# Kernel tuning notes

Measured on AMD Instinct MI355X. Metric: run time of the kernel, lower is better.

Reference implementation:

```python
import jax, jax.numpy as jnp
import numpy as np
import math

L, D, H, V, B, S, MR = 8, 768, 12, 32000, 2, 1024, 4
HD = D // H

def setup_inputs() -> dict:
    key = jax.random.key(0)
    ks = iter(jax.random.split(key, 64))
    def rn(shape, s=0.02):
        return jax.random.normal(next(ks), shape, jnp.float32) * s
    inp = {}
    inp['tokens'] = jax.random.randint(next(ks), (B, S), 0, V, jnp.int32)
    inp['tok_emb'] = rn((V, D))
    inp['pos_emb'] = rn((S, D))
    for n in ['Wq_row', 'Wk_row', 'Wv_row', 'Wq_col', 'Wo']:
        inp[n] = rn((L, D, D))
    for n in ['bq_row', 'bk_row', 'bv_row', 'bq_col', 'bo']:
        inp[n] = jnp.zeros((L, D), jnp.float32)
    inp['ln1_g'] = jnp.ones((L, D), jnp.float32); inp['ln1_b'] = jnp.zeros((L, D), jnp.float32)
    inp['ln2_g'] = jnp.ones((L, D), jnp.float32); inp['ln2_b'] = jnp.zeros((L, D), jnp.float32)
    inp['W1'] = rn((L, D, MR * D)); inp['b1'] = jnp.zeros((L, MR * D), jnp.float32)
    inp['W2'] = rn((L, MR * D, D)); inp['b2'] = jnp.zeros((L, D), jnp.float32)
    inp['Wk_sh'] = rn((D, D)); inp['bk_sh'] = jnp.zeros((D,), jnp.float32)
    inp['Wv_sh'] = rn((D, D)); inp['bv_sh'] = jnp.zeros((D,), jnp.float32)
    inp['lnf_g'] = jnp.ones((D,), jnp.float32); inp['lnf_b'] = jnp.zeros((D,), jnp.float32)
    inp['Whead'] = rn((D, V)); inp['bhead'] = jnp.zeros((V,), jnp.float32)
    return inp

def _ln(x, g, b, eps=1e-5):
    m = x.mean(-1, keepdims=True)
    v = ((x - m) ** 2).mean(-1, keepdims=True)
    return (x - m) * jax.lax.rsqrt(v + eps) * g + b

def _heads(x):
    b, s, _ = x.shape
    return x.reshape(b, s, H, HD).transpose(0, 2, 1, 3)  # [B,H,S,hd]

def _merge(x):
    b, h, s, hd = x.shape
    return x.transpose(0, 2, 1, 3).reshape(b, s, h * hd)

def _forward(tokens, tok_emb, pos_emb, Wq_row, bq_row, Wk_row, bk_row, Wv_row, bv_row,
             Wq_col, bq_col, Wo, bo, ln1_g, ln1_b, ln2_g, ln2_b, W1, b1, W2, b2,
             Wk_sh, bk_sh, Wv_sh, bv_sh, lnf_g, lnf_b, Whead, bhead):
    s_len = tokens.shape[1]
    inv = 1.0 / math.sqrt(HD)
    x = tok_emb[tokens] + pos_emb[:s_len]
    mask = jnp.triu(jnp.ones((s_len, s_len), bool), 1)
    past_k, past_v = [], []
    for i in range(L):
        h = _ln(x, ln1_g[i], ln1_b[i])
        q_row = _heads(h @ Wq_row[i] + bq_row[i])
        k_row = _heads(h @ Wk_row[i] + bk_row[i])
        v_row = _heads(h @ Wv_row[i] + bv_row[i])
        q_col = _heads(h @ Wq_col[i] + bq_col[i])
        k_col = _heads(h @ Wk_sh + bk_sh)   # shared KV projector (archived memory)
        v_col = _heads(h @ Wv_sh + bv_sh)
        ts = jnp.einsum('bhqd,bhkd->bhqk', q_row, k_row) * inv
        ts = jnp.where(mask, -jnp.inf, ts)
        if past_k:
            pk = jnp.stack(past_k, axis=3)  # [B,H,S,l,hd]
            pv = jnp.stack(past_v, axis=3)
            ms = jnp.einsum('bhsd,bhsld->bhsl', q_col, pk) * inv
            w = jax.nn.softmax(jnp.concatenate([ts, ms], axis=-1), axis=-1)
            tw, mw = w[..., :s_len], w[..., s_len:]
            ctx = (jnp.einsum('bhqk,bhkd->bhqd', tw, v_row)
                   + jnp.einsum('bhsl,bhsld->bhsd', mw, pv))
        else:
            ctx = jnp.einsum('bhqk,bhkd->bhqd', jax.nn.softmax(ts, axis=-1), v_row)
        x = x + (_merge(ctx) @ Wo[i] + bo[i])
        h2 = _ln(x, ln2_g[i], ln2_b[i])
        x = x + (jax.nn.gelu(h2 @ W1[i] + b1[i], approximate=False) @ W2[i] + b2[i])
        past_k.append(k_col)
        past_v.append(v_col)
    return _ln(x, lnf_g, lnf_b) @ Whead + bhead

def reference(tokens, tok_emb, pos_emb, Wq_row, bq_row, Wk_row, bk_row, Wv_row, bv_row,
              Wq_col, bq_col, Wo, bo, ln1_g, ln1_b, ln2_g, ln2_b, W1, b1, W2, b2,
              Wk_sh, bk_sh, Wv_sh, bv_sh, lnf_g, lnf_b, Whead, bhead):
    return _forward(tokens, tok_emb, pos_emb, Wq_row, bq_row, Wk_row, bk_row, Wv_row, bv_row,
                    Wq_col, bq_col, Wo, bo, ln1_g, ln1_b, ln2_g, ln2_b, W1, b1, W2, b2,
                    Wk_sh, bk_sh, Wv_sh, bv_sh, lnf_g, lnf_b, Whead, bhead)
```

## Files before the change

### kernel.cpp

```cpp
#include <hip/hip_runtime.h>
#include <hip/hip_bf16.h>
#include <math.h>

#define L_   8
#define D_   768
#define H_   12
#define V_   32000
#define B_   2
#define S_   1024
#define HD_  64
#define BS_  2048
#define DFF_ 3072

typedef __hip_bfloat16 bf16;
typedef __attribute__((ext_vector_type(8))) short bf16x8;
typedef __attribute__((ext_vector_type(4))) float f32x4;

#define CFUN(r) (((r) >> 1) & 3)

__device__ __forceinline__ void cp16(void* lds, const void* g) {
  __builtin_amdgcn_global_load_lds(
      (const __attribute__((address_space(1))) void*)g,
      (__attribute__((address_space(3))) void*)lds, 16, 0, 0);
}

__device__ __forceinline__ unsigned short f2bf(float v) {
  __hip_bfloat16 h = __float2bfloat16(v);
  return *reinterpret_cast<unsigned short*>(&h);
}
__device__ __forceinline__ float bf2f(unsigned short u) {
  return __uint_as_float(((unsigned)u) << 16);
}

__global__ __launch_bounds__(256) void k_embed(const int* __restrict__ tokens,
    const float* __restrict__ tok_emb, const float* __restrict__ pos_emb,
    float* __restrict__ x) {
  int idx = blockIdx.x * 256 + threadIdx.x;
  int row = idx / D_;
  int d   = idx - row * D_;
  int s   = row & (S_ - 1);
  int t   = tokens[row];
  x[idx] = tok_emb[(size_t)t * D_ + d] + pos_emb[(size_t)s * D_ + d];
}

__global__ __launch_bounds__(256) void k_ln(const float* __restrict__ x,
    const float* __restrict__ g, const float* __restrict__ b,
    bf16* __restrict__ out) {
  int row = blockIdx.x;
  const float* xr = x + (size_t)row * D_;
  int t = threadIdx.x;
  float v0 = xr[t], v1 = xr[t + 256], v2 = xr[t + 512];
  float s  = v0 + v1 + v2;
  float s2 = v0 * v0 + v1 * v1 + v2 * v2;
#pragma unroll
  for (int off = 32; off; off >>= 1) {
    s  += __shfl_down(s, off);
    s2 += __shfl_down(s2, off);
  }
  __shared__ float rs[4], rs2[4];
  __shared__ float mean_s, rstd_s;
  int wid = t >> 6;
  if ((t & 63) == 0) { rs[wid] = s; rs2[wid] = s2; }
  __syncthreads();
  if (t == 0) {
    float S1 = rs[0] + rs[1] + rs[2] + rs[3];
    float S2 = rs2[0] + rs2[1] + rs2[2] + rs2[3];
    float m  = S1 / D_;
    float var = S2 / D_ - m * m;
    mean_s = m;
    rstd_s = rsqrtf(var + 1e-5f);
  }
  __syncthreads();
  float m = mean_s, r = rstd_s;
  bf16* orow = out + (size_t)row * D_;
  orow[t]       = __float2bfloat16((v0 - m) * r * g[t]       + b[t]);
  orow[t + 256] = __float2bfloat16((v1 - m) * r * g[t + 256] + b[t + 256]);
  orow[t + 512] = __float2bfloat16((v2 - m) * r * g[t + 512] + b[t + 512]);
}

__global__ __launch_bounds__(256) void k_w2bf_t(const float* __restrict__ W,
    bf16* __restrict__ Wt, int K, int N, size_t ils, size_t ols) {
  __shared__ float t[32][33];
  const float* Wm = W + (size_t)blockIdx.z * ils;
  bf16* Wtm = Wt + (size_t)blockIdx.z * ols;
  int n0 = blockIdx.x * 32, k0 = blockIdx.y * 32;
  int tx = threadIdx.x;
  for (int i = threadIdx.y; i < 32; i += 8)
    t[i][tx] = Wm[(size_t)(k0 + i) * N + n0 + tx];
  __syncthreads();
  for (int i = threadIdx.y; i < 32; i += 8)
    Wtm[(size_t)(n0 + i) * K + k0 + tx] = __float2bfloat16(t[tx][i]);
}

__global__ __launch_bounds__(256) void k_bcat(const float* __restrict__ bq,
    const float* __restrict__ bk, const float* __restrict__ bqc,
    const float* __restrict__ bv, const float* __restrict__ bksh,
    const float* __restrict__ bvsh, float* __restrict__ b6) {
  int idx = blockIdx.x * 256 + threadIdx.x;
  if (idx >= L_ * 4608) return;
  int l = idx / 4608, c = idx - l * 4608;
  float v = (c < 768)  ? bq[l * 768 + c]
          : (c < 1536) ? bk[l * 768 + c - 768]
          : (c < 2304) ? bqc[l * 768 + c - 1536]
          : (c < 3072) ? bv[l * 768 + c - 2304]
          : (c < 3840) ? bksh[c - 3072]
                       : bvsh[c - 3840];
  b6[idx] = v;
}

template <int BM, int EPI>
__global__ __launch_bounds__(256) void k_bgemm(
    const bf16* __restrict__ A, const bf16* __restrict__ Wt,
    const float* __restrict__ bias, const float* __restrict__ resid,
    float* __restrict__ Cf, bf16* __restrict__ Cb, bf16* __restrict__ Cb2,
    bf16* __restrict__ Cb3, int NM, int M, int N, int K) {
  constexpr int ASZ = BM * 64;
  constexpr int ALINES = BM / 64;
  constexpr int BSTRIDE = ASZ + 8192;
  constexpr int MF = BM / 32;
  __shared__ __align__(16) char smem[3 * BSTRIDE];
  const int tid = threadIdx.x;
  const int l = tid & 63, w = tid >> 6;
  const int wr = w >> 1, wc = w & 1;

  const int nwg = (int)gridDim.x;
  int id = (int)blockIdx.x;
  id = (id & 7) * (nwg >> 3) + (id >> 3);
  const int m0 = (id % NM) * BM;
  const int n0 = (id / NM) * 128;

  const int lane15 = l & 15, lg = l >> 4;

  const int r0 = tid >> 2, p0 = tid & 3;
  const char* aSrc[ALINES];
#pragma unroll
  for (int i = 0; i < ALINES; i++) {
    const int rr = i * 64 + r0;
    aSrc[i] = (const char*)(A + (size_t)(m0 + rr) * K) + ((p0 ^ CFUN(rr)) * 16);
  }
  const char* bSrc0 = (const char*)(Wt + (size_t)(n0 + r0) * K) + ((p0 ^ CFUN(r0)) * 16);
  const char* bSrc1 = (const char*)(Wt + (size_t)(n0 + 64 + r0) * K) + ((p0 ^ CFUN(64 + r0)) * 16);

  int aOff[MF], bOff[4];
#pragma unroll
  for (int mi = 0; mi < MF; mi++) {
    int r = wr * (BM / 2) + mi * 16 + lane15;
    aOff[mi] = r * 64 + ((lg ^ CFUN(r)) * 16);
  }
#pragma unroll
  for (int ni = 0; ni < 4; ni++) {
    int r = wc * 64 + ni * 16 + lane15;
    bOff[ni] = ASZ + r * 64 + ((lg ^ CFUN(r)) * 16);
  }

  f32x4 acc[MF][4];
#pragma unroll
  for (int mi = 0; mi < MF; mi++)
#pragma unroll
    for (int ni = 0; ni < 4; ni++) acc[mi][ni] = (f32x4){0.f, 0.f, 0.f, 0.f};

  auto stage = [&](int buf, int t) {
    const size_t kb = (size_t)t * 64;
    char* base = smem + buf * BSTRIDE;
#pragma unroll
    for (int i = 0; i < ALINES; i++)
      cp16(base + i * 4096 + w * 1024, aSrc[i] + kb);
    cp16(base + ASZ + w * 1024, bSrc0 + kb);
    cp16(base + ASZ + 4096 + w * 1024, bSrc1 + kb);
  };
  auto compute = [&](int buf) {
    const char* base = smem + buf * BSTRIDE;
    bf16x8 af[MF], bfr[4];
#pragma unroll
    for (int mi = 0; mi < MF; mi++) af[mi] = *(const bf16x8*)(base + aOff[mi]);
#pragma unroll
    for (int ni = 0; ni < 4; ni++) bfr[ni] = *(const bf16x8*)(base + bOff[ni]);
    __builtin_amdgcn_s_setprio(1);
#pragma unroll
    for (int mi = 0; mi < MF; mi++)
#pragma unroll
      for (int ni = 0; ni < 4; ni++)
        acc[mi][ni] = __builtin_amdgcn_mfma_f32_16x16x32_bf16(
            af[mi], bfr[ni], acc[mi][ni], 0, 0, 0);
    __builtin_amdgcn_s_setprio(0);
  };

  const int nk = K >> 5;
  stage(0, 0);
  stage(1, 1);
  int buf = 0;
  for (int t = 0; t < nk; t++) {
    if (t + 1 < nk) {
      if constexpr (ALINES == 2) asm volatile("s_waitcnt vmcnt(4)" ::: "memory");
      else                       asm volatile("s_waitcnt vmcnt(3)" ::: "memory");
    } else {
      asm volatile("s_waitcnt vmcnt(0)" ::: "memory");
    }
    __builtin_amdgcn_s_barrier();
    if (t + 2 < nk) {
      int nb = buf + 2; if (nb >= 3) nb -= 3;
      stage(nb, t + 2);
    }
    compute(buf);
    buf = (buf == 2) ? 0 : buf + 1;
  }

#pragma unroll
  for (int ni = 0; ni < 4; ni++) {
    const int col = n0 + wc * 64 + ni * 16 + lane15;
    const float bv = bias[col];
#pragma unroll
    for (int mi = 0; mi < MF; mi++) {
      const int rowb = m0 + wr * (BM / 2) + mi * 16 + lg * 4;
      if constexpr (EPI == 6) {
        if (col < 2304) {
#pragma unroll
          for (int j = 0; j < 4; j++)
            Cb[(size_t)(rowb + j) * 2304 + col] = __float2bfloat16(acc[mi][ni][j] + bv);
        } else if (col < 3072) {
          ushort4 pk;
          pk.x = f2bf(acc[mi][ni][0] + bv);
          pk.y = f2bf(acc[mi][ni][1] + bv);
          pk.z = f2bf(acc[mi][ni][2] + bv);
          pk.w = f2bf(acc[mi][ni][3] + bv);
          const int bq = rowb >> 10, s = rowb & (S_ - 1);
          *reinterpret_cast<ushort4*>(
              (unsigned short*)Cb2 + ((size_t)(bq * 768 + (col - 2304))) * S_ + s) = pk;
        } else {
#pragma unroll
          for (int j = 0; j < 4; j++)
            Cb3[(size_t)(rowb + j) * 1536 + (col - 3072)] =
                __float2bfloat16(acc[mi][ni][j] + bv);
        }
      } else {
#pragma unroll
        for (int j = 0; j < 4; j++) {
          const int row = rowb + j;
          float v = acc[mi][ni][j] + bv;
          if constexpr (EPI == 1) v += resid[(size_t)row * N + col];
          if constexpr (EPI == 2) {
            v = 0.5f * v * (1.0f + erff(v * 0.70710678118654752f));
            Cb[(size_t)row * N + col] = __float2bfloat16(v);
          } else if constexpr (EPI == 3) {
            Cb[(size_t)row * N + col] = __float2bfloat16(v);
          } else {
            Cf[(size_t)row * N + col] = v;
          }
        }
      }
    }
  }
}

__global__ __launch_bounds__(256) void k_attn(
    const bf16* __restrict__ qkv, const bf16* __restrict__ vT,
    const bf16* __restrict__ memkv, bf16* __restrict__ ctx, int layer) {
  const int bh = blockIdx.x;
  const int b = bh / H_, h = bh % H_;
  const int qt = (int)gridDim.y - 1 - (int)blockIdx.y;
  const int tid = threadIdx.x;
  const int w = tid >> 6, l = tid & 63;
  const int lane15 = l & 15, lg = l >> 4;
  const float inv = 0.125f;

  __shared__ char plds[4][2048];
  __shared__ float wlp[4][16][16];
  char* pl = plds[w];

  const int qrow0 = qt * 64 + w * 16;
  const size_t rowA = (size_t)(b * S_ + qrow0 + lane15);
  const bf16* qp = qkv + rowA * 2304 + h * 64 + lg * 8;
  const bf16x8 qf0 = *(const bf16x8*)(qp);
  const bf16x8 qf1 = *(const bf16x8*)(qp + 32);

  const bf16* kbase = qkv + (size_t)(b * S_) * 2304 + 768 + h * 64 + lg * 8;
  const bf16* vbase = vT + ((size_t)(b * 768 + h * 64 + lane15)) * S_;

  float mrow[4], dsum[4];
  f32x4 acc[4];
#pragma unroll
  for (int j = 0; j < 4; j++) { mrow[j] = -INFINITY; dsum[j] = 0.f; }
#pragma unroll
  for (int ni = 0; ni < 4; ni++) acc[ni] = (f32x4){0.f, 0.f, 0.f, 0.f};

  const int ntile = ((qrow0 + 15) >> 6) + 1;
  for (int kt64 = 0; kt64 < ntile; kt64++) {
    const int k0 = kt64 * 64;
    f32x4 sc[4];
#pragma unroll
    for (int kt = 0; kt < 4; kt++) {
      const bf16* kp = kbase + (size_t)(k0 + kt * 16 + lane15) * 2304;
      bf16x8 kf0 = *(const bf16x8*)(kp);
      bf16x8 kf1 = *(const bf16x8*)(kp + 32);
      f32x4 z = (f32x4){0.f, 0.f, 0.f, 0.f};
      z = __builtin_amdgcn_mfma_f32_16x16x32_bf16(qf0, kf0, z, 0, 0, 0);
      sc[kt] = __builtin_amdgcn_mfma_f32_16x16x32_bf16(qf1, kf1, z, 0, 0, 0);
    }
    float tmax[4];
#pragma unroll
    for (int j = 0; j < 4; j++) tmax[j] = -INFINITY;
#pragma unroll
    for (int kt = 0; kt < 4; kt++) {
      const int kabs = k0 + kt * 16 + lane15;
#pragma unroll
      for (int j = 0; j < 4; j++) {
        const int qabs = qrow0 + lg * 4 + j;
        float v = (kabs <= qabs) ? sc[kt][j] * inv : -INFINITY;
        sc[kt][j] = v;
        tmax[j] = fmaxf(tmax[j], v);
      }
    }
#pragma unroll
    for (int off = 1; off < 16; off <<= 1)
#pragma unroll
      for (int j = 0; j < 4; j++) tmax[j] = fmaxf(tmax[j], __shfl_xor(tmax[j], off, 16));

    float psum[4];
#pragma unroll
    for (int j = 0; j < 4; j++) {
      const float mnew = fmaxf(mrow[j], tmax[j]);
      const float alpha = __expf(mrow[j] - mnew);
      mrow[j] = mnew;
      dsum[j] *= alpha;
#pragma unroll
      for (int ni = 0; ni < 4; ni++) acc[ni][j] *= alpha;
      psum[j] = 0.f;
    }
#pragma unroll
    for (int kt = 0; kt < 4; kt++) {
      const int gsl = kt * 2 + (lane15 >> 3);
      const int ebyte = (lane15 & 7) * 2;
#pragma unroll
      for (int j = 0; j < 4; j++) {
        const float p = __expf(sc[kt][j] - mrow[j]);
        psum[j] += p;
        const int r = lg * 4 + j;
        *(unsigned short*)(pl + r * 128 + ((gsl ^ (r & 7)) << 4) + ebyte) = f2bf(p);
      }
    }
#pragma unroll
    for (int off = 1; off < 16; off <<= 1)
#pragma unroll
      for (int j = 0; j < 4; j++) psum[j] += __shfl_xor(psum[j], off, 16);
#pragma unroll
    for (int j = 0; j < 4; j++) dsum[j] += psum[j];

#pragma unroll
    for (int ks = 0; ks < 2; ks++) {
      bf16x8 pa = *(const bf16x8*)(pl + lane15 * 128 +
                                   ((((ks << 2) + lg) ^ (lane15 & 7)) << 4));
      const bf16* vp = vbase + k0 + ks * 32 + lg * 8;
#pragma unroll
      for (int ni = 0; ni < 4; ni++) {
        bf16x8 vf = *(const bf16x8*)(vp + (size_t)ni * 16 * S_);
        acc[ni] = __builtin_amdgcn_mfma_f32_16x16x32_bf16(pa, vf, acc[ni], 0, 0, 0);
      }
    }
  }

  const int r4 = lg * 4;
  if (lane15 < layer) {
    const int ml = lane15;
#pragma unroll
    for (int j = 0; j < 4; j++) {
      const size_t rowB = (size_t)(b * S_) + qrow0 + r4 + j;
      const bf16* qc = qkv + rowB * 2304 + 1536 + h * 64;
      const bf16* mk = memkv + ((size_t)ml * BS_ + rowB) * 1536 + h * 64;
      float d_ = 0.f;
#pragma unroll
      for (int t = 0; t < 8; t++) {
        bf16x8 qv = *(const bf16x8*)(qc + t * 8);
        bf16x8 kv = *(const bf16x8*)(mk + t * 8);
#pragma unroll
        for (int e = 0; e < 8; e++)
          d_ += bf2f((unsigned short)qv[e]) * bf2f((unsigned short)kv[e]);
      }
      wlp[w][r4 + j][ml] = d_ * inv;
    }
  }
  if (layer > 0) {
#pragma unroll
    for (int j = 0; j < 4; j++) {
      const int r = r4 + j;
      float mm = -INFINITY;
      for (int ml = 0; ml < layer; ml++) mm = fmaxf(mm, wlp[w][r][ml]);
      const float mnew = fmaxf(mrow[j], mm);
      const float alpha = __expf(mrow[j] - mnew);
      mrow[j] = mnew;
      dsum[j] *= alpha;
#pragma unroll
      for (int ni = 0; ni < 4; ni++) acc[ni][j] *= alpha;
      const size_t rowB = (size_t)(b * S_) + qrow0 + r;
      for (int ml = 0; ml < layer; ml++) {
        const float p = __expf(wlp[w][r][ml] - mnew);
        dsum[j] += p;
        const unsigned short* mv = (const unsigned short*)(memkv +
            ((size_t)ml * BS_ + rowB) * 1536 + 768 + h * 64 + lane15);
#pragma unroll
        for (int ni = 0; ni < 4; ni++)
          acc[ni][j] += p * bf2f(mv[ni * 16]);
      }
    }
  }

#pragma unroll
  for (int j = 0; j < 4; j++) {
    const float rd = 1.f / dsum[j];
    const size_t rowB = (size_t)(b * S_) + qrow0 + r4 + j;
    bf16* cp = ctx + rowB * 768 + h * 64 + lane15;
#pragma unroll
    for (int ni = 0; ni < 4; ni++)
      cp[ni * 16] = __float2bfloat16(acc[ni][j] * rd);
  }
}

extern "C" void kernel_launch(void* const* d_in, const int* in_sizes, int n_in,
                              void* d_out, int out_size, void* d_ws, size_t ws_size,
                              hipStream_t stream) {
  const int*   tokens  = (const int*)d_in[0];
  const float* tok_emb = (const float*)d_in[1];
  const float* pos_emb = (const float*)d_in[2];
  const float *Wq_row, *Wk_row, *Wv_row, *Wq_col, *Wo;
  const float *bq_row, *bk_row, *bv_row, *bq_col, *bo;
  if (in_sizes[4] == L_ * D_ * D_) {
    Wq_row = (const float*)d_in[3];  Wk_row = (const float*)d_in[4];
    Wv_row = (const float*)d_in[5];  Wq_col = (const float*)d_in[6];
    Wo     = (const float*)d_in[7];
    bq_row = (const float*)d_in[8];  bk_row = (const float*)d_in[9];
    bv_row = (const float*)d_in[10]; bq_col = (const float*)d_in[11];
    bo     = (const float*)d_in[12];
  } else {
    Wq_row = (const float*)d_in[3];  bq_row = (const float*)d_in[4];
    Wk_row = (const float*)d_in[5];  bk_row = (const float*)d_in[6];
    Wv_row = (const float*)d_in[7];  bv_row = (const float*)d_in[8];
    Wq_col = (const float*)d_in[9];  bq_col = (const float*)d_in[10];
    Wo     = (const float*)d_in[11]; bo     = (const float*)d_in[12];
  }
  const float* ln1_g = (const float*)d_in[13]; const float* ln1_b = (const float*)d_in[14];
  const float* ln2_g = (const float*)d_in[15]; const float* ln2_b = (const float*)d_in[16];
  const float* W1    = (const float*)d_in[17]; const float* b1    = (const float*)d_in[18];
  const float* W2    = (const float*)d_in[19]; const float* b2    = (const float*)d_in[20];
  const float* Wk_sh = (const float*)d_in[21]; const float* bk_sh = (const float*)d_in[22];
  const float* Wv_sh = (const float*)d_in[23]; const float* bv_sh = (const float*)d_in[24];
  const float* lnf_g = (const float*)d_in[25]; const float* lnf_b = (const float*)d_in[26];
  const float* Whead = (const float*)d_in[27]; const float* bhead = (const float*)d_in[28];

  char* p = (char*)d_ws;
  float* x      = (float*)p; p += (size_t)BS_ * D_ * 4;
  bf16*  h_bf   = (bf16*)p;  p += (size_t)BS_ * D_ * 2;
  bf16*  qkv3   = (bf16*)p;  p += (size_t)BS_ * 2304 * 2;
  bf16*  vTb    = (bf16*)p;  p += (size_t)B_ * 768 * S_ * 2;
  bf16*  memkv  = (bf16*)p;  p += (size_t)L_ * BS_ * 1536 * 2;
  bf16*  ctx_bf = (bf16*)p;  p += (size_t)BS_ * D_ * 2;
  bf16*  mlp_bf = (bf16*)p;  p += (size_t)BS_ * DFF_ * 2;
  float* b6cat  = (float*)p; p += (size_t)L_ * 4608 * 4;
  bf16* tW6    = (bf16*)p; p += (size_t)L_ * 4608 * D_ * 2;
  bf16* tWo    = (bf16*)p; p += (size_t)L_ * D_ * D_ * 2;
  bf16* tW1    = (bf16*)p; p += (size_t)L_ * DFF_ * D_ * 2;
  bf16* tW2    = (bf16*)p; p += (size_t)L_ * D_ * DFF_ * 2;
  bf16* tWhead = (bf16*)p; p += (size_t)V_ * D_ * 2;

  dim3 tb(32, 8);
  const size_t DD = (size_t)D_ * D_;
  const size_t W6S = (size_t)4608 * 768;
  k_w2bf_t<<<dim3(24, 24, L_), tb, 0, stream>>>(Wq_row, tW6,              768, 768, DD, W6S);
  k_w2bf_t<<<dim3(24, 24, L_), tb, 0, stream>>>(Wk_row, tW6 + 768 * 768,  768, 768, DD, W6S);
  k_w2bf_t<<<dim3(24, 24, L_), tb, 0, stream>>>(Wq_col, tW6 + 1536 * 768, 768, 768, DD, W6S);
  k_w2bf_t<<<dim3(24, 24, L_), tb, 0, stream>>>(Wv_row, tW6 + 2304 * 768, 768, 768, DD, W6S);
  k_w2bf_t<<<dim3(24, 24, L_), tb, 0, stream>>>(Wk_sh,  tW6 + 3072 * 768, 768, 768, 0, W6S);
  k_w2bf_t<<<dim3(24, 24, L_), tb, 0, stream>>>(Wv_sh,  tW6 + 3840 * 768, 768, 768, 0, W6S);
  k_w2bf_t<<<dim3(24, 24, L_), tb, 0, stream>>>(Wo,     tWo, 768, 768, DD, DD);
  k_w2bf_t<<<dim3(96, 24, L_), tb, 0, stream>>>(W1, tW1, 768, 3072, (size_t)768 * 3072, (size_t)3072 * 768);
  k_w2bf_t<<<dim3(24, 96, L_), tb, 0, stream>>>(W2, tW2, 3072, 768, (size_t)768 * 3072, (size_t)768 * 3072);
  k_w2bf_t<<<dim3(1000, 24, 1), tb, 0, stream>>>(Whead, tWhead, 768, 32000, 0, 0);
  k_bcat<<<dim3(144), 256, 0, stream>>>(bq_row, bk_row, bq_col, bv_row, bk_sh, bv_sh, b6cat);

  k_embed<<<dim3((BS_ * D_) / 256), 256, 0, stream>>>(tokens, tok_emb, pos_emb, x);

  for (int i = 0; i < L_; i++) {
    k_ln<<<dim3(BS_), 256, 0, stream>>>(x, ln1_g + i * D_, ln1_b + i * D_, h_bf);
    k_bgemm<128, 6><<<dim3(576), 256, 0, stream>>>(
        h_bf, tW6 + (size_t)i * W6S, b6cat + (size_t)i * 4608,
        nullptr, nullptr, qkv3, vTb, memkv + (size_t)i * BS_ * 1536,
        16, BS_, 4608, 768);
    k_attn<<<dim3(B_ * H_, S_ / 64), 256, 0, stream>>>(qkv3, vTb, memkv, ctx_bf, i);
    k_bgemm<64, 1><<<dim3(192), 256, 0, stream>>>(
        ctx_bf, tWo + (size_t)i * DD, bo + i * D_, x, x, nullptr, nullptr, nullptr,
        32, BS_, 768, 768);
    k_ln<<<dim3(BS_), 256, 0, stream>>>(x, ln2_g + i * D_, ln2_b + i * D_, h_bf);
    k_bgemm<128, 2><<<dim3(384), 256, 0, stream>>>(
        h_bf, tW1 + (size_t)i * 3072 * 768, b1 + (size_t)i * DFF_,
        nullptr, nullptr, mlp_bf, nullptr, nullptr, 16, BS_, 3072, 768);
    k_bgemm<64, 1><<<dim3(192), 256, 0, stream>>>(
        mlp_bf, tW2 + (size_t)i * 768 * 3072, b2 + i * D_, x, x, nullptr, nullptr,
        nullptr, 32, BS_, 768, 3072);
  }
  k_ln<<<dim3(BS_), 256, 0, stream>>>(x, lnf_g, lnf_b, h_bf);
  k_bgemm<128, 0><<<dim3(4000), 256, 0, stream>>>(
      h_bf, tWhead, bhead, nullptr, (float*)d_out, nullptr, nullptr, nullptr,
      16, BS_, V_, 768);
}
```

Baseline: 1.876 ms.

## Add dedicated 256x256-tile ping-pong GEMM kernel for LM head projection

Replaces the generic 128-tile GEMM for the final vocab projection with a specialized 512-thread kernel using 256x256 output tiles, double-buffered LDS loaded via global_load_lds, XOR-swizzled layout, and interleaved MFMA/load phases with barriers and s_setprio. The larger tile raises arithmetic intensity and reduces redundant A/B traffic, and the block index remap improves L2 locality. It uses 128KB LDS at one block per CU, hard-codes the K=768 and N=32000 shapes, and 1000 blocks on a chip with many CUs may leave a tail.

```diff
diff --git a/kernel.cpp b/kernel.cpp
--- a/kernel.cpp
+++ b/kernel.cpp
@@ -248,6 +248,158 @@
           }
         }
       }
+    }
+  }
+}
+
+#define HBAR() asm volatile("s_barrier" ::: "memory")
+#define MFMA16(AF, BF, MB, NB)                                               \
+  do {                                                                       \
+    __builtin_amdgcn_s_setprio(1);                                           \
+    _Pragma("unroll") for (int mi_ = 0; mi_ < 4; mi_++)                      \
+      _Pragma("unroll") for (int ni_ = 0; ni_ < 2; ni_++)                    \
+        _Pragma("unroll") for (int ks_ = 0; ks_ < 2; ks_++)                  \
+          acc[(MB) + mi_][(NB) + ni_] =                                      \
+              __builtin_amdgcn_mfma_f32_16x16x32_bf16(                       \
+                  AF[mi_][ks_], BF[ni_][ks_], acc[(MB) + mi_][(NB) + ni_],   \
+                  0, 0, 0);                                                  \
+    __builtin_amdgcn_s_setprio(0);                                           \
+  } while (0)
+
+__global__ __launch_bounds__(512, 1) void k_head8(const bf16* __restrict__ A,
+    const bf16* __restrict__ Wt, const float* __restrict__ bias,
+    float* __restrict__ C) {
+  __shared__ __align__(16) char smem[131072];
+  const int tid = threadIdx.x;
+  const int l = tid & 63, w = tid >> 6;
+  const int wr = w >> 2, wc = w & 3;
+  const int lane15 = l & 15, lg = l >> 4;
+
+  int id = (int)blockIdx.x;
+  id = (id & 7) * 125 + (id >> 3);
+  const int m0 = (id % 8) * 256;
+  const int n0 = (id / 8) * 256;
+
+  auto issueA = [&](int tile, int hb) {
+#pragma unroll
+    for (int j = 0; j < 2; j++) {
+      const int idx = j * 512 + tid;
+      const int rl = idx >> 3, sl = idx & 7;
+      const bf16* g = A + (size_t)(m0 + hb + rl) * 768 + tile * 64 +
+                      ((sl ^ (rl & 7)) << 3);
+      cp16(smem + (tile & 1) * 32768 + hb * 128 + (j * 512 + w * 64) * 16, g);
+    }
+  };
+  auto issueB = [&](int tile, int hb) {
+#pragma unroll
+    for (int j = 0; j < 2; j++) {
+      const int idx = j * 512 + tid;
+      const int rl = idx >> 3, sl = idx & 7;
+      const bf16* g = Wt + (size_t)(n0 + hb + rl) * 768 + tile * 64 +
+                      ((sl ^ (rl & 7)) << 3);
+      cp16(smem + 65536 + (tile & 1) * 32768 + hb * 128 + (j * 512 + w * 64) * 16, g);
+    }
+  };
+  auto ldA = [&](int buf, int mi, int ks) {
+    const int r = wr * 128 + mi * 16 + lane15;
+    return *(const bf16x8*)(smem + buf * 32768 + r * 128 +
+                            ((((ks << 2) + lg) ^ (r & 7)) << 4));
+  };
+  auto ldB = [&](int buf, int ni, int ks) {
+    const int r = wc * 64 + ni * 16 + lane15;
+    return *(const bf16x8*)(smem + 65536 + buf * 32768 + r * 128 +
+                            ((((ks << 2) + lg) ^ (r & 7)) << 4));
+  };
+
+  f32x4 acc[8][4];
+#pragma unroll
+  for (int i = 0; i < 8; i++)
+#pragma unroll
+    for (int j = 0; j < 4; j++) acc[i][j] = (f32x4){0.f, 0.f, 0.f, 0.f};
+  bf16x8 alo[4][2], ahi[4][2], blo[2][2], bhi[2][2];
+
+  issueA(0, 0);  issueA(0, 128);  issueB(0, 0);  issueB(0, 128);
+  issueB(1, 0);  issueA(1, 0);    issueB(1, 128);
+  asm volatile("s_waitcnt vmcnt(6)" ::: "memory");
+  HBAR();
+
+  for (int it = 0; it < 5; ++it) {
+    const int Tb = 2 * it + 1, Tn = 2 * it + 2;
+#pragma unroll
+    for (int mi = 0; mi < 4; mi++) { alo[mi][0] = ldA(0, mi, 0); alo[mi][1] = ldA(0, mi, 1); }
+#pragma unroll
+    for (int ni = 0; ni < 2; ni++) { blo[ni][0] = ldB(0, ni, 0); blo[ni][1] = ldB(0, ni, 1); }
+    issueA(Tb, 128);
+    HBAR(); MFMA16(alo, blo, 0, 0); HBAR();
+#pragma unroll
+    for (int ni = 0; ni < 2; ni++) { bhi[ni][0] = ldB(0, ni + 2, 0); bhi[ni][1] = ldB(0, ni + 2, 1); }
+    HBAR(); MFMA16(alo, bhi, 0, 2); HBAR();
+#pragma unroll
+    for (int mi = 0; mi < 4; mi++) { ahi[mi][0] = ldA(0, mi + 4, 0); ahi[mi][1] = ldA(0, mi + 4, 1); }
+    issueB(Tn, 0);
+    HBAR(); MFMA16(ahi, bhi, 4, 2); HBAR();
+    issueA(Tn, 0);
+    issueB(Tn, 128);
+    asm volatile("s_waitcnt vmcnt(6)" ::: "memory");
+    HBAR(); MFMA16(ahi, blo, 4, 0); HBAR();
+#pragma unroll
+    for (int mi = 0; mi < 4; mi++) { alo[mi][0] = ldA(1, mi, 0); alo[mi][1] = ldA(1, mi, 1); }
+#pragma unroll
+    for (int ni = 0; ni < 2; ni++) { blo[ni][0] = ldB(1, ni, 0); blo[ni][1] = ldB(1, ni, 1); }
+    issueA(Tn, 128);
+    HBAR(); MFMA16(alo, blo, 0, 0); HBAR();
+#pragma unroll
+    for (int ni = 0; ni < 2; ni++) { bhi[ni][0] = ldB(1, ni + 2, 0); bhi[ni][1] = ldB(1, ni + 2, 1); }
+    HBAR(); MFMA16(alo, bhi, 0, 2); HBAR();
+#pragma unroll
+    for (int mi = 0; mi < 4; mi++) { ahi[mi][0] = ldA(1, mi + 4, 0); ahi[mi][1] = ldA(1, mi + 4, 1); }
+    issueB(Tn + 1, 0);
+    HBAR(); MFMA16(ahi, bhi, 4, 2); HBAR();
+    issueA(Tn + 1, 0);
+    issueB(Tn + 1, 128);
+    asm volatile("s_waitcnt vmcnt(6)" ::: "memory");
+    HBAR(); MFMA16(ahi, blo, 4, 0); HBAR();
+  }
+
+  {
+#pragma unroll
+    for (int mi = 0; mi < 4; mi++) { alo[mi][0] = ldA(0, mi, 0); alo[mi][1] = ldA(0, mi, 1); }
+#pragma unroll
+    for (int ni = 0; ni < 2; ni++) { blo[ni][0] = ldB(0, ni, 0); blo[ni][1] = ldB(0, ni, 1); }
+    issueA(11, 128);
+    HBAR(); MFMA16(alo, blo, 0, 0); HBAR();
+#pragma unroll
+    for (int ni = 0; ni < 2; ni++) { bhi[ni][0] = ldB(0, ni + 2, 0); bhi[ni][1] = ldB(0, ni + 2, 1); }
+    HBAR(); MFMA16(alo, bhi, 0, 2); HBAR();
+#pragma unroll
+    for (int mi = 0; mi < 4; mi++) { ahi[mi][0] = ldA(0, mi + 4, 0); ahi[mi][1] = ldA(0, mi + 4, 1); }
+    HBAR(); MFMA16(ahi, bhi, 4, 2); HBAR();
+    asm volatile("s_waitcnt vmcnt(0)" ::: "memory");
+    HBAR(); MFMA16(ahi, blo, 4, 0); HBAR();
+#pragma unroll
+    for (int mi = 0; mi < 4; mi++) { alo[mi][0] = ldA(1, mi, 0); alo[mi][1] = ldA(1, mi, 1); }
+#pragma unroll
+    for (int ni = 0; ni < 2; ni++) { blo[ni][0] = ldB(1, ni, 0); blo[ni][1] = ldB(1, ni, 1); }
+    MFMA16(alo, blo, 0, 0);
+#pragma unroll
+    for (int ni = 0; ni < 2; ni++) { bhi[ni][0] = ldB(1, ni + 2, 0); bhi[ni][1] = ldB(1, ni + 2, 1); }
+    MFMA16(alo, bhi, 0, 2);
+#pragma unroll
+    for (int mi = 0; mi < 4; mi++) { ahi[mi][0] = ldA(1, mi + 4, 0); ahi[mi][1] = ldA(1, mi + 4, 1); }
+    MFMA16(ahi, bhi, 4, 2);
+    MFMA16(ahi, blo, 4, 0);
+  }
+
+#pragma unroll
+  for (int ni = 0; ni < 4; ni++) {
+    const int col = n0 + wc * 64 + ni * 16 + lane15;
+    const float bv = bias[col];
+#pragma unroll
+    for (int mi = 0; mi < 8; mi++) {
+      const int rowb = m0 + wr * 128 + mi * 16 + lg * 4;
+#pragma unroll
+      for (int j = 0; j < 4; j++)
+        C[(size_t)(rowb + j) * 32000 + col] = acc[mi][ni][j] + bv;
     }
   }
 }
@@ -496,7 +648,5 @@
         nullptr, 32, BS_, 768, 3072);
   }
   k_ln<<<dim3(BS_), 256, 0, stream>>>(x, lnf_g, lnf_b, h_bf);
-  k_bgemm<128, 0><<<dim3(4000), 256, 0, stream>>>(
-      h_bf, tWhead, bhead, nullptr, (float*)d_out, nullptr, nullptr, nullptr,
-      16, BS_, V_, 768);
-}
+  k_head8<<<dim3(1000), 512, 0, stream>>>(h_bf, tWhead, bhead, (float*)d_out);
+}
```

New measurement: 1.844 ms. About the same (-1.7%).
